# Kernel tuning notes

Hardware: AMD Instinct MI355X
Metric: run time of the kernel (lower is better)

The kernel has to match this reference:

```python
import jax, jax.numpy as jnp
import numpy as np

NEG_SLOPE = 0.01  # nn.LeakyReLU default
NUM_GRAPHS = 64


def leaky_relu(x):
    return jnp.where(x >= 0, x, NEG_SLOPE * x)


def gcn_conv(x, edge_index, W, b):
    """PyG GCNConv: add self-loops, symmetric norm, aggregate, + bias."""
    n = x.shape[0]
    h = x @ W  # [N, F]
    loop = jnp.arange(n, dtype=edge_index.dtype)
    src = jnp.concatenate([edge_index[0], loop])
    dst = jnp.concatenate([edge_index[1], loop])
    deg = jax.ops.segment_sum(jnp.ones_like(dst, dtype=h.dtype), dst, num_segments=n)
    dinv = jnp.where(deg > 0, deg ** -0.5, 0.0)
    norm = dinv[src] * dinv[dst]  # [E+N]
    msg = h[src] * norm[:, None]  # [E+N, F] dominant intermediate
    out = jax.ops.segment_sum(msg, dst, num_segments=n)
    return out + b


def gep(x, batch, num_graphs):
    """global mean pool over batch segment ids."""
    s = jax.ops.segment_sum(x, batch, num_segments=num_graphs)
    cnt = jax.ops.segment_sum(jnp.ones(x.shape[0], dtype=x.dtype), batch, num_segments=num_graphs)
    return s / jnp.maximum(cnt, 1.0)[:, None]


def setup_inputs() -> dict:
    key = jax.random.key(0)
    ks = jax.random.split(key, 16)
    N, E, F, D, B = 10000, 80000, 1024, 128, NUM_GRAPHS
    sc = 1.0 / np.sqrt(F)
    inp = {
        "pro1_x": jax.random.normal(ks[0], (N, F), jnp.float32),
        "pro1_edge_index": jax.random.randint(ks[1], (2, E), 0, N, jnp.int64),
        "pro1_batch": jnp.sort(jax.random.randint(ks[2], (N,), 0, B, jnp.int64)),
        "pro2_x": jax.random.normal(ks[3], (N, F), jnp.float32),
        "pro2_edge_index": jax.random.randint(ks[4], (2, E), 0, N, jnp.int64),
        "pro2_batch": jnp.sort(jax.random.randint(ks[5], (N,), 0, B, jnp.int64)),
        "mas1_straight": 0, "mas1_flipped": 0, "mas2_straight": 0, "mas2_flipped": 0,
        "conv1_W": jax.random.normal(ks[6], (F, F), jnp.float32) * sc,
        "conv1_b": jnp.zeros((F,), jnp.float32),
        "fc1_W": jax.random.normal(ks[7], (F, D), jnp.float32) * sc,
        "fc1_b": jnp.zeros((D,), jnp.float32),
        "conv2_W": jax.random.normal(ks[8], (F, F), jnp.float32) * sc,
        "conv2_b": jnp.zeros((F,), jnp.float32),
        "fc2_W": jax.random.normal(ks[9], (F, D), jnp.float32) * sc,
        "fc2_b": jnp.zeros((D,), jnp.float32),
        "final_W": jax.random.normal(ks[10], (2 * D, 1), jnp.float32) * (1.0 / np.sqrt(2 * D)),
        "final_b": jnp.zeros((1,), jnp.float32),
    }
    return inp


def reference(pro1_x, pro1_edge_index, pro1_batch, pro2_x, pro2_edge_index, pro2_batch,
              mas1_straight, mas1_flipped, mas2_straight, mas2_flipped,
              conv1_W, conv1_b, fc1_W, fc1_b, conv2_W, conv2_b, fc2_W, fc2_b,
              final_W, final_b):
    # branch 1 (dropout = identity at inference)
    x = leaky_relu(gcn_conv(pro1_x, pro1_edge_index, conv1_W, conv1_b))
    x = gep(x, pro1_batch, NUM_GRAPHS)
    x = leaky_relu(x @ fc1_W + fc1_b)
    # branch 2
    xt = leaky_relu(gcn_conv(pro2_x, pro2_edge_index, conv2_W, conv2_b))
    xt = gep(xt, pro2_batch, NUM_GRAPHS)
    xt = leaky_relu(xt @ fc2_W + fc2_b)
    combined = jnp.concatenate([x, xt], axis=1)  # [B, 256]
    return combined @ final_W + final_b  # [B, 1]
```

## Files before the change

kernel.cpp:

```cpp
#include <hip/hip_runtime.h>
#include <cstdint>
#include <cstddef>

#define FDIM 1024
#define DDIM 128
#define NGRAPH 64
#define FCH 8
#define QN 4

#define AS1 __attribute__((address_space(1)))
#define AS3 __attribute__((address_space(3)))

typedef float f32x4 __attribute__((ext_vector_type(4)));
typedef short s16x8 __attribute__((ext_vector_type(8)));

__device__ __forceinline__ unsigned short f2bf(float f) {
  unsigned int x = __float_as_uint(f);
  unsigned int r = (x + 0x7fffu + ((x >> 16) & 1u)) >> 16;
  return (unsigned short)r;
}
__device__ __forceinline__ float bf2f(unsigned short u) {
  return __uint_as_float(((unsigned int)u) << 16);
}
__device__ __forceinline__ float bflo(unsigned int v) {
  return __uint_as_float(v << 16);
}
__device__ __forceinline__ float bfhi(unsigned int v) {
  return __uint_as_float(v & 0xffff0000u);
}

__device__ __forceinline__ int lower_bound(const int* a, int n, int v) {
  int lo = 0, hi = n;
  while (lo < hi) {
    int mid = (lo + hi) >> 1;
    if (a[mid] < v) lo = mid + 1; else hi = mid;
  }
  return lo;
}
__global__ __launch_bounds__(256) void k_init_cnt(float4* pool1, float4* pool2,
                                                  int* deg1, int* deg2,
                                                  const int* __restrict__ batch1,
                                                  const int* __restrict__ batch2,
                                                  int* cnt1, int* gstart1,
                                                  int* cnt2, int* gstart2, int N) {
  int bid = blockIdx.x, t = threadIdx.x;
  const float4 z = make_float4(0.f, 0.f, 0.f, 0.f);
  if (bid < 64) {
    pool1[bid * 256 + t] = z;
  } else if (bid < 128) {
    pool2[(bid - 64) * 256 + t] = z;
  } else if (bid < 168) {
    int i = (bid - 128) * 256 + t;
    if (i < N) deg1[i] = 1;
  } else if (bid < 208) {
    int i = (bid - 168) * 256 + t;
    if (i < N) deg2[i] = 1;
  } else {
    if (t < 128) {
      const int* batch = (t < NGRAPH) ? batch1 : batch2;
      int* cnt = (t < NGRAPH) ? cnt1 : cnt2;
      int* gstart = (t < NGRAPH) ? gstart1 : gstart2;
      int g = t & (NGRAPH - 1);
      int lo = lower_bound(batch, N, g);
      int hi = lower_bound(batch, N, g + 1);
      gstart[g] = lo;
      cnt[g] = hi - lo;
    }
  }
}

__global__ void k_prep(const int* __restrict__ ei1, const int* __restrict__ ei2,
                       int* deg1, int* deg2, int E) {
  const int* ei = blockIdx.y ? ei2 : ei1;
  int* deg = blockIdx.y ? deg2 : deg1;
  int i = blockIdx.x * blockDim.x + threadIdx.x;
  if (i < E) atomicAdd(&deg[ei[E + i]], 1);
}

#define SCAN_T 1024
#define SCAN_PER 16
__global__ __launch_bounds__(SCAN_T) void k_scan(const int* __restrict__ deg1,
                                                 const int* __restrict__ deg2,
                                                 int* off1, int* off2,
                                                 int* cur1, int* cur2,
                                                 float* dinv1, float* dinv2, int n) {
  const int* deg = blockIdx.x ? deg2 : deg1;
  int* off = blockIdx.x ? off2 : off1;
  int* cur = blockIdx.x ? cur2 : cur1;
  float* dinv = blockIdx.x ? dinv2 : dinv1;
  __shared__ int sums[SCAN_T];
  int t = threadIdx.x;
  int base = t * SCAN_PER;
  int local[SCAN_PER];
  int s = 0;
  #pragma unroll
  for (int i = 0; i < SCAN_PER; ++i) {
    int idx = base + i;
    int d = (idx < n) ? deg[idx] : 0;
    local[i] = s;
    s += d;
    if (idx < n) dinv[idx] = rsqrtf((float)d);
  }
  sums[t] = s;
  __syncthreads();
  for (int o = 1; o < SCAN_T; o <<= 1) {
    int v = (t >= o) ? sums[t - o] : 0;
    __syncthreads();
    sums[t] += v;
    __syncthreads();
  }
  int basesum = (t > 0) ? sums[t - 1] : 0;
  #pragma unroll
  for (int i = 0; i < SCAN_PER; ++i) {
    int idx = base + i;
    if (idx < n) { int o = basesum + local[i]; off[idx] = o; cur[idx] = o; }
  }
  if (t == SCAN_T - 1) off[n] = sums[SCAN_T - 1];
}

__global__ void k_fill(const int* __restrict__ ei1, const int* __restrict__ ei2,
                       int* cur1, int* cur2,
                       const float* __restrict__ dinv1, const float* __restrict__ dinv2,
                       int* adjsrc1, int* adjsrc2,
                       float* adjw1, float* adjw2, int E, int N) {
  const int* ei = blockIdx.y ? ei2 : ei1;
  int* cur = blockIdx.y ? cur2 : cur1;
  const float* dinv = blockIdx.y ? dinv2 : dinv1;
  int* adjsrc = blockIdx.y ? adjsrc2 : adjsrc1;
  float* adjw = blockIdx.y ? adjw2 : adjw1;
  int i = blockIdx.x * blockDim.x + threadIdx.x;
  if (i < E) {
    int s = ei[i];
    int d = ei[E + i];
    int p = atomicAdd(&cur[d], 1);
    adjsrc[p] = s;
    adjw[p] = dinv[s] * dinv[d];
  }
  if (i < N) {
    int p = atomicAdd(&cur[i], 1);
    adjsrc[p] = i;
    adjw[p] = dinv[i] * dinv[i];
  }
}

__global__ __launch_bounds__(256) void k_cast(const float4* __restrict__ x1,
                                              const float4* __restrict__ x2,
                                              const float* __restrict__ W1,
                                              const float* __restrict__ W2,
                                              ushort4* xb1, ushort4* xb2,
                                              unsigned short* Wt1, unsigned short* Wt2,
                                              int n4, int nxb) {
  __shared__ unsigned short tile[64][65];
  int bid = blockIdx.x, t = threadIdx.x;
  if (bid < 2 * nxb) {
    int br = bid >= nxb;
    const float4* x = br ? x2 : x1;
    ushort4* xb = br ? xb2 : xb1;
    int i = (bid - br * nxb) * 256 + t;
    if (i < n4) {
      float4 v = x[i];
      ushort4 o;
      o.x = f2bf(v.x); o.y = f2bf(v.y); o.z = f2bf(v.z); o.w = f2bf(v.w);
      xb[i] = o;
    }
  } else {
    int w = bid - 2 * nxb;
    int br = w >= 256;
    const float* W = br ? W2 : W1;
    unsigned short* Wt = br ? Wt2 : Wt1;
    int tid16 = w - br * 256;
    int kb = tid16 >> 4, nb = tid16 & 15;
    int tn = t & 63, tg = t >> 6;
    #pragma unroll
    for (int r = 0; r < 16; ++r) {
      int kk = tg * 16 + r;
      tile[kk][tn] = f2bf(W[(size_t)(kb * 64 + kk) * FDIM + nb * 64 + tn]);
    }
    __syncthreads();
    #pragma unroll
    for (int r = 0; r < 16; ++r) {
      int nn = tg * 16 + r;
      Wt[(size_t)(nb * 64 + nn) * FDIM + kb * 64 + tn] = tile[tn][nn];
    }
  }
}

__global__ __launch_bounds__(256) void k_gemm_bf16(const unsigned short* __restrict__ A1,
                                                   const unsigned short* __restrict__ A2,
                                                   const unsigned short* __restrict__ B1,
                                                   const unsigned short* __restrict__ B2,
                                                   unsigned short* __restrict__ C1,
                                                   unsigned short* __restrict__ C2,
                                                   int M) {
  const unsigned short* A = blockIdx.y ? A2 : A1;
  const unsigned short* Bt = blockIdx.y ? B2 : B1;
  unsigned short* C = blockIdx.y ? C2 : C1;
  const int K = FDIM;
  __shared__ unsigned short sm[8192];
  int tid = threadIdx.x;
  int w = tid >> 6, lane = tid & 63;
  int wm = w >> 1, wn = w & 1;

  int per_xcd = gridDim.x >> 3;
  int l = (blockIdx.x & 7) * per_xcd + (blockIdx.x >> 3);
  int m0 = (l >> 3) * 128;
  int n0 = (l & 7) * 128;

  int sub = lane >> 2;
  int kq = lane & 3;

  f32x4 acc[4][4];
  #pragma unroll
  for (int i = 0; i < 4; ++i)
    #pragma unroll
    for (int j = 0; j < 4; ++j)
      acc[i][j] = (f32x4){0.f, 0.f, 0.f, 0.f};

  for (int k0 = 0; k0 < K; k0 += 32) {
    #pragma unroll
    for (int j = 0; j < 2; ++j) {
      int chunk = w * 2 + j;
      int ra = m0 + chunk * 16 + sub;
      if (ra > M - 1) ra = M - 1;
      const unsigned short* ga = A + (size_t)ra * K + k0 + kq * 8;
      __builtin_amdgcn_global_load_lds((const AS1 unsigned int*)ga,
                                       (AS3 unsigned int*)&sm[chunk * 512], 16, 0, 0);
      int rb = n0 + chunk * 16 + sub;
      const unsigned short* gb = Bt + (size_t)rb * K + k0 + kq * 8;
      __builtin_amdgcn_global_load_lds((const AS1 unsigned int*)gb,
                                       (AS3 unsigned int*)&sm[4096 + chunk * 512], 16, 0, 0);
    }
    __syncthreads();
    s16x8 af[4], bfr[4];
    #pragma unroll
    for (int i = 0; i < 4; ++i) {
      int rowa = wm * 64 + i * 16 + (lane & 15);
      af[i] = *(const s16x8*)&sm[rowa * 32 + (lane >> 4) * 8];
      int rowb = wn * 64 + i * 16 + (lane & 15);
      bfr[i] = *(const s16x8*)&sm[4096 + rowb * 32 + (lane >> 4) * 8];
    }
    #pragma unroll
    for (int i = 0; i < 4; ++i)
      #pragma unroll
      for (int j = 0; j < 4; ++j)
        acc[i][j] = __builtin_amdgcn_mfma_f32_16x16x32_bf16(af[i], bfr[j], acc[i][j], 0, 0, 0);
    __syncthreads();
  }

  #pragma unroll
  for (int i = 0; i < 4; ++i) {
    int row_base = m0 + wm * 64 + i * 16 + (lane >> 4) * 4;
    #pragma unroll
    for (int j = 0; j < 4; ++j) {
      int col = n0 + wn * 64 + j * 16 + (lane & 15);
      #pragma unroll
      for (int r = 0; r < 4; ++r) {
        int row = row_base + r;
        if (row < M) C[(size_t)row * FDIM + col] = f2bf(acc[i][j][r]);
      }
    }
  }
}

__global__ __launch_bounds__(256) void k_aggpool(const unsigned short* __restrict__ h1,
                                                 const unsigned short* __restrict__ h2,
                                                 const int* __restrict__ off1,
                                                 const int* __restrict__ off2,
                                                 const int* __restrict__ adjsrc1,
                                                 const int* __restrict__ adjsrc2,
                                                 const float* __restrict__ adjw1,
                                                 const float* __restrict__ adjw2,
                                                 const float* __restrict__ bias1,
                                                 const float* __restrict__ bias2,
                                                 const int* __restrict__ cnt1,
                                                 const int* __restrict__ cnt2,
                                                 const int* __restrict__ gstart1,
                                                 const int* __restrict__ gstart2,
                                                 float* pool1, float* pool2) {
  int br = blockIdx.y;
  const unsigned short* h = br ? h2 : h1;
  const int* off = br ? off2 : off1;
  const int* adjsrc = br ? adjsrc2 : adjsrc1;
  const float* adjw = br ? adjw2 : adjw1;
  const float* bias = br ? bias2 : bias1;
  const int* cnt = br ? cnt2 : cnt1;
  const int* gstart = br ? gstart2 : gstart1;
  float* pool = br ? pool2 : pool1;

  int x = blockIdx.x;
  int chunk = x & (FCH - 1);
  int r = x >> 3;
  int g = r & (NGRAPH - 1);
  int q = r >> 6;

  int t = threadIdx.x;
  int grp = t >> 6, lane = t & 63;

  int n = cnt[g];
  int start = gstart[g];
  int per = (n + QN - 1) / QN;
  int v0 = start + q * per;
  int v1 = min(start + n, v0 + per);

  int colbase = chunk * 128 + lane * 2;
  const unsigned short* hc = h + colbase;
  float2 b2 = *(const float2*)(bias + colbase);
  float s0 = 0.f, s1 = 0.f;

  for (int v = v0 + grp; v < v1; v += 4) {
    int pb = off[v], pe = off[v + 1];
    float a0 = 0.f, a1 = 0.f;
    for (int pbb = pb; pbb < pe; pbb += 64) {
      int m = min(64, pe - pbb);
      int lp = pbb + ((lane < m) ? lane : (m - 1));
      int vs = adjsrc[lp];
      float vw = adjw[lp];
      int j = 0;
      for (; j + 4 <= m; j += 4) {
        int i0 = __shfl(vs, j),     i1 = __shfl(vs, j + 1);
        int i2 = __shfl(vs, j + 2), i3 = __shfl(vs, j + 3);
        float w0 = __shfl(vw, j),     w1 = __shfl(vw, j + 1);
        float w2 = __shfl(vw, j + 2), w3 = __shfl(vw, j + 3);
        unsigned int h0 = *(const unsigned int*)(hc + ((size_t)i0 << 10));
        unsigned int hv1 = *(const unsigned int*)(hc + ((size_t)i1 << 10));
        unsigned int hv2 = *(const unsigned int*)(hc + ((size_t)i2 << 10));
        unsigned int hv3 = *(const unsigned int*)(hc + ((size_t)i3 << 10));
        a0 += w0 * bflo(h0);  a1 += w0 * bfhi(h0);
        a0 += w1 * bflo(hv1); a1 += w1 * bfhi(hv1);
        a0 += w2 * bflo(hv2); a1 += w2 * bfhi(hv2);
        a0 += w3 * bflo(hv3); a1 += w3 * bfhi(hv3);
      }
      for (; j < m; ++j) {
        int i0 = __shfl(vs, j);
        float w0 = __shfl(vw, j);
        unsigned int h0 = *(const unsigned int*)(hc + ((size_t)i0 << 10));
        a0 += w0 * bflo(h0);
        a1 += w0 * bfhi(h0);
      }
    }
    a0 += b2.x; a1 += b2.y;
    s0 += (a0 >= 0.f) ? a0 : 0.01f * a0;
    s1 += (a1 >= 0.f) ? a1 : 0.01f * a1;
  }

  __shared__ float sm[4][128];
  sm[grp][lane * 2] = s0;
  sm[grp][lane * 2 + 1] = s1;
  __syncthreads();
  if (t < 128) {
    float sum = sm[0][t] + sm[1][t] + sm[2][t] + sm[3][t];
    float ic = 1.0f / fmaxf((float)n, 1.0f);
    atomicAdd(pool + (size_t)g * FDIM + chunk * 128 + t, sum * ic);
  }
}

__global__ __launch_bounds__(DDIM) void k_fc(const float* __restrict__ pool1,
                                             const float* __restrict__ pool2,
                                             const float* __restrict__ W1,
                                             const float* __restrict__ W2,
                                             const float* __restrict__ b1,
                                             const float* __restrict__ b2,
                                             float* out1, float* out2) {
  const float* pool = blockIdx.y ? pool2 : pool1;
  const float* W = blockIdx.y ? W2 : W1;
  const float* b = blockIdx.y ? b2 : b1;
  float* out = blockIdx.y ? out2 : out1;
  int g = blockIdx.x;
  int j = threadIdx.x;
  __shared__ float xs[FDIM];
  for (int k = j; k < FDIM; k += DDIM) xs[k] = pool[(size_t)g * FDIM + k];
  __syncthreads();
  float acc = b[j];
  for (int k = 0; k < FDIM; ++k) acc += xs[k] * W[(size_t)k * DDIM + j];
  out[g * DDIM + j] = (acc >= 0.f) ? acc : 0.01f * acc;
}

__global__ __launch_bounds__(DDIM) void k_final(const float* __restrict__ o1,
                                                const float* __restrict__ o2,
                                                const float* __restrict__ W,
                                                const float* __restrict__ b,
                                                float* __restrict__ out) {
  int g = blockIdx.x;
  int t = threadIdx.x;
  float acc = o1[g * DDIM + t] * W[t] + o2[g * DDIM + t] * W[DDIM + t];
  #pragma unroll
  for (int o = 32; o > 0; o >>= 1) acc += __shfl_down(acc, o);
  __shared__ float ws2[2];
  if ((t & 63) == 0) ws2[t >> 6] = acc;
  __syncthreads();
  if (t == 0) out[g] = ws2[0] + ws2[1] + b[0];
}

extern "C" void kernel_launch(void* const* d_in, const int* in_sizes, int n_in,
                              void* d_out, int out_size, void* d_ws, size_t ws_size,
                              hipStream_t stream) {
  const float* x1 = (const float*)d_in[0];
  const int* ei1 = (const int*)d_in[1];
  const int* batch1 = (const int*)d_in[2];
  const float* x2 = (const float*)d_in[3];
  const int* ei2 = (const int*)d_in[4];
  const int* batch2 = (const int*)d_in[5];
  const float* conv1_W = (const float*)d_in[10];
  const float* conv1_b = (const float*)d_in[11];
  const float* fc1_W = (const float*)d_in[12];
  const float* fc1_b = (const float*)d_in[13];
  const float* conv2_W = (const float*)d_in[14];
  const float* conv2_b = (const float*)d_in[15];
  const float* fc2_W = (const float*)d_in[16];
  const float* fc2_b = (const float*)d_in[17];
  const float* final_W = (const float*)d_in[18];
  const float* final_b = (const float*)d_in[19];
  float* out = (float*)d_out;

  const int N = in_sizes[2];
  const int E = in_sizes[1] / 2;
  const int A = E + N;

  size_t off_b = 0;
  auto alloc = [&](size_t bytes) -> void* {
    void* p = (char*)d_ws + off_b;
    off_b += (bytes + 255) & ~(size_t)255;
    return p;
  };
  unsigned short* xbf1 = (unsigned short*)alloc((size_t)N * FDIM * 2);
  unsigned short* xbf2 = (unsigned short*)alloc((size_t)N * FDIM * 2);
  unsigned short* hbf1 = (unsigned short*)alloc((size_t)N * FDIM * 2);
  unsigned short* hbf2 = (unsigned short*)alloc((size_t)N * FDIM * 2);
  unsigned short* Wt1 = (unsigned short*)alloc((size_t)FDIM * FDIM * 2);
  unsigned short* Wt2 = (unsigned short*)alloc((size_t)FDIM * FDIM * 2);
  int* deg1 = (int*)alloc(N * 4);
  int* deg2 = (int*)alloc(N * 4);
  int* cnt1 = (int*)alloc(NGRAPH * 4);
  int* cnt2 = (int*)alloc(NGRAPH * 4);
  int* gstart1 = (int*)alloc(NGRAPH * 4);
  int* gstart2 = (int*)alloc(NGRAPH * 4);
  int* off1 = (int*)alloc((N + 1) * 4);
  int* off2 = (int*)alloc((N + 1) * 4);
  int* cur1 = (int*)alloc(N * 4);
  int* cur2 = (int*)alloc(N * 4);
  float* dinv1 = (float*)alloc(N * 4);
  float* dinv2 = (float*)alloc(N * 4);
  int* adjsrc1 = (int*)alloc((size_t)A * 4);
  int* adjsrc2 = (int*)alloc((size_t)A * 4);
  float* adjw1 = (float*)alloc((size_t)A * 4);
  float* adjw2 = (float*)alloc((size_t)A * 4);
  float* pool1 = (float*)alloc(NGRAPH * FDIM * 4);
  float* pool2 = (float*)alloc(NGRAPH * FDIM * 4);
  float* fco1 = (float*)alloc(NGRAPH * DDIM * 4);
  float* fco2 = (float*)alloc(NGRAPH * DDIM * 4);

  const int T = 256;
  int gE = (E + T - 1) / T;
  int n4 = N * FDIM / 4;
  int nxb = (n4 + T - 1) / T;
  int mt = (N + 127) / 128;
  dim3 gGemm(mt * 8, 2);
  dim3 gPrep(gE, 2);
  dim3 gAgg(FCH * NGRAPH * QN, 2);
  dim3 gFc(NGRAPH, 2);

  k_init_cnt<<<209, T, 0, stream>>>((float4*)pool1, (float4*)pool2, deg1, deg2,
                                    batch1, batch2, cnt1, gstart1, cnt2, gstart2, N);
  k_prep<<<gPrep, T, 0, stream>>>(ei1, ei2, deg1, deg2, E);
  k_scan<<<2, SCAN_T, 0, stream>>>(deg1, deg2, off1, off2, cur1, cur2, dinv1, dinv2, N);
  k_fill<<<gPrep, T, 0, stream>>>(ei1, ei2, cur1, cur2, dinv1, dinv2,
                                  adjsrc1, adjsrc2, adjw1, adjw2, E, N);
  k_cast<<<2 * nxb + 512, T, 0, stream>>>((const float4*)x1, (const float4*)x2,
                                          conv1_W, conv2_W,
                                          (ushort4*)xbf1, (ushort4*)xbf2, Wt1, Wt2,
                                          n4, nxb);
  k_gemm_bf16<<<gGemm, 256, 0, stream>>>(xbf1, xbf2, Wt1, Wt2, hbf1, hbf2, N);
  k_aggpool<<<gAgg, 256, 0, stream>>>(hbf1, hbf2, off1, off2, adjsrc1, adjsrc2,
                                      adjw1, adjw2, conv1_b, conv2_b,
                                      cnt1, cnt2, gstart1, gstart2, pool1, pool2);
  k_fc<<<gFc, DDIM, 0, stream>>>(pool1, pool2, fc1_W, fc2_W, fc1_b, fc2_b, fco1, fco2);
  k_final<<<NGRAPH, DDIM, 0, stream>>>(fco1, fco2, final_W, final_b, out);
}
```

Baseline: 340.5 us.

## Merge prep/cast and fill/gemm launches; replace pool atomics with per-quarter partials

Folds the degree-count atomics into the cast kernel and the CSR fill into the GEMM launch as extra leading blocks, which removes two kernel launches and lets the independent work run concurrently. The pooled-sum atomics are replaced by per-quarter partial buffers that k_fc reduces, so the pool zeroing in the init kernel can be dropped. The cost is larger grids with divergent block roles, a fixed FILLB block count that must cover E (320 blocks of 256 ≥ 80000), and extra partial-buffer memory.

```diff
diff --git a/kernel.cpp b/kernel.cpp
--- a/kernel.cpp
+++ b/kernel.cpp
@@ -7,6 +7,7 @@
 #define NGRAPH 64
 #define FCH 8
 #define QN 4
+#define FILLB 320
 
 #define AS1 __attribute__((address_space(1)))
 #define AS3 __attribute__((address_space(3)))
@@ -18,9 +19,6 @@
   unsigned int x = __float_as_uint(f);
   unsigned int r = (x + 0x7fffu + ((x >> 16) & 1u)) >> 16;
   return (unsigned short)r;
-}
-__device__ __forceinline__ float bf2f(unsigned short u) {
-  return __uint_as_float(((unsigned int)u) << 16);
 }
 __device__ __forceinline__ float bflo(unsigned int v) {
   return __uint_as_float(v << 16);
@@ -37,23 +35,17 @@
   }
   return lo;
 }
-__global__ __launch_bounds__(256) void k_init_cnt(float4* pool1, float4* pool2,
-                                                  int* deg1, int* deg2,
-                                                  const int* __restrict__ batch1,
-                                                  const int* __restrict__ batch2,
-                                                  int* cnt1, int* gstart1,
-                                                  int* cnt2, int* gstart2, int N) {
+__global__ __launch_bounds__(256) void k_init(int* deg1, int* deg2,
+                                              const int* __restrict__ batch1,
+                                              const int* __restrict__ batch2,
+                                              int* cnt1, int* gstart1,
+                                              int* cnt2, int* gstart2, int N) {
   int bid = blockIdx.x, t = threadIdx.x;
-  const float4 z = make_float4(0.f, 0.f, 0.f, 0.f);
-  if (bid < 64) {
-    pool1[bid * 256 + t] = z;
-  } else if (bid < 128) {
-    pool2[(bid - 64) * 256 + t] = z;
-  } else if (bid < 168) {
-    int i = (bid - 128) * 256 + t;
+  if (bid < 40) {
+    int i = bid * 256 + t;
     if (i < N) deg1[i] = 1;
-  } else if (bid < 208) {
-    int i = (bid - 168) * 256 + t;
+  } else if (bid < 80) {
+    int i = (bid - 40) * 256 + t;
     if (i < N) deg2[i] = 1;
   } else {
     if (t < 128) {
@@ -69,12 +61,52 @@
   }
 }
 
-__global__ void k_prep(const int* __restrict__ ei1, const int* __restrict__ ei2,
-                       int* deg1, int* deg2, int E) {
-  const int* ei = blockIdx.y ? ei2 : ei1;
-  int* deg = blockIdx.y ? deg2 : deg1;
-  int i = blockIdx.x * blockDim.x + threadIdx.x;
-  if (i < E) atomicAdd(&deg[ei[E + i]], 1);
+__global__ __launch_bounds__(256) void k_prep_cast(const int* __restrict__ ei1,
+                                                   const int* __restrict__ ei2,
+                                                   int* deg1, int* deg2,
+                                                   const float4* __restrict__ x1,
+                                                   const float4* __restrict__ x2,
+                                                   const float* __restrict__ W1,
+                                                   const float* __restrict__ W2,
+                                                   ushort4* xb1, ushort4* xb2,
+                                                   unsigned short* Wt1, unsigned short* Wt2,
+                                                   int E, int n4, int gE, int nxb) {
+  __shared__ unsigned short tile[64][65];
+  int br = blockIdx.y;
+  int x = blockIdx.x, t = threadIdx.x;
+  if (x < gE) {
+    const int* ei = br ? ei2 : ei1;
+    int* deg = br ? deg2 : deg1;
+    int i = x * 256 + t;
+    if (i < E) atomicAdd(&deg[ei[E + i]], 1);
+  } else if (x < gE + nxb) {
+    const float4* xx = br ? x2 : x1;
+    ushort4* xb = br ? xb2 : xb1;
+    int i = (x - gE) * 256 + t;
+    if (i < n4) {
+      float4 v = xx[i];
+      ushort4 o;
+      o.x = f2bf(v.x); o.y = f2bf(v.y); o.z = f2bf(v.z); o.w = f2bf(v.w);
+      xb[i] = o;
+    }
+  } else {
+    const float* W = br ? W2 : W1;
+    unsigned short* Wt = br ? Wt2 : Wt1;
+    int tid16 = x - gE - nxb;
+    int kb = tid16 >> 4, nb = tid16 & 15;
+    int tn = t & 63, tg = t >> 6;
+    #pragma unroll
+    for (int r = 0; r < 16; ++r) {
+      int kk = tg * 16 + r;
+      tile[kk][tn] = f2bf(W[(size_t)(kb * 64 + kk) * FDIM + nb * 64 + tn]);
+    }
+    __syncthreads();
+    #pragma unroll
+    for (int r = 0; r < 16; ++r) {
+      int nn = tg * 16 + r;
+      Wt[(size_t)(nb * 64 + nn) * FDIM + kb * 64 + tn] = tile[tn][nn];
+    }
+  }
 }
 
 #define SCAN_T 1024
@@ -118,91 +150,54 @@
   if (t == SCAN_T - 1) off[n] = sums[SCAN_T - 1];
 }
 
-__global__ void k_fill(const int* __restrict__ ei1, const int* __restrict__ ei2,
-                       int* cur1, int* cur2,
-                       const float* __restrict__ dinv1, const float* __restrict__ dinv2,
-                       int* adjsrc1, int* adjsrc2,
-                       float* adjw1, float* adjw2, int E, int N) {
-  const int* ei = blockIdx.y ? ei2 : ei1;
-  int* cur = blockIdx.y ? cur2 : cur1;
-  const float* dinv = blockIdx.y ? dinv2 : dinv1;
-  int* adjsrc = blockIdx.y ? adjsrc2 : adjsrc1;
-  float* adjw = blockIdx.y ? adjw2 : adjw1;
-  int i = blockIdx.x * blockDim.x + threadIdx.x;
-  if (i < E) {
-    int s = ei[i];
-    int d = ei[E + i];
-    int p = atomicAdd(&cur[d], 1);
-    adjsrc[p] = s;
-    adjw[p] = dinv[s] * dinv[d];
-  }
-  if (i < N) {
-    int p = atomicAdd(&cur[i], 1);
-    adjsrc[p] = i;
-    adjw[p] = dinv[i] * dinv[i];
-  }
-}
-
-__global__ __launch_bounds__(256) void k_cast(const float4* __restrict__ x1,
-                                              const float4* __restrict__ x2,
-                                              const float* __restrict__ W1,
-                                              const float* __restrict__ W2,
-                                              ushort4* xb1, ushort4* xb2,
-                                              unsigned short* Wt1, unsigned short* Wt2,
-                                              int n4, int nxb) {
-  __shared__ unsigned short tile[64][65];
-  int bid = blockIdx.x, t = threadIdx.x;
-  if (bid < 2 * nxb) {
-    int br = bid >= nxb;
-    const float4* x = br ? x2 : x1;
-    ushort4* xb = br ? xb2 : xb1;
-    int i = (bid - br * nxb) * 256 + t;
-    if (i < n4) {
-      float4 v = x[i];
-      ushort4 o;
-      o.x = f2bf(v.x); o.y = f2bf(v.y); o.z = f2bf(v.z); o.w = f2bf(v.w);
-      xb[i] = o;
-    }
-  } else {
-    int w = bid - 2 * nxb;
-    int br = w >= 256;
-    const float* W = br ? W2 : W1;
-    unsigned short* Wt = br ? Wt2 : Wt1;
-    int tid16 = w - br * 256;
-    int kb = tid16 >> 4, nb = tid16 & 15;
-    int tn = t & 63, tg = t >> 6;
-    #pragma unroll
-    for (int r = 0; r < 16; ++r) {
-      int kk = tg * 16 + r;
-      tile[kk][tn] = f2bf(W[(size_t)(kb * 64 + kk) * FDIM + nb * 64 + tn]);
-    }
-    __syncthreads();
-    #pragma unroll
-    for (int r = 0; r < 16; ++r) {
-      int nn = tg * 16 + r;
-      Wt[(size_t)(nb * 64 + nn) * FDIM + kb * 64 + tn] = tile[tn][nn];
-    }
-  }
-}
-
-__global__ __launch_bounds__(256) void k_gemm_bf16(const unsigned short* __restrict__ A1,
+__global__ __launch_bounds__(256) void k_fill_gemm(const int* __restrict__ ei1,
+                                                   const int* __restrict__ ei2,
+                                                   int* cur1, int* cur2,
+                                                   const float* __restrict__ dinv1,
+                                                   const float* __restrict__ dinv2,
+                                                   int* adjsrc1, int* adjsrc2,
+                                                   float* adjw1, float* adjw2,
+                                                   const unsigned short* __restrict__ A1,
                                                    const unsigned short* __restrict__ A2,
                                                    const unsigned short* __restrict__ B1,
                                                    const unsigned short* __restrict__ B2,
                                                    unsigned short* __restrict__ C1,
                                                    unsigned short* __restrict__ C2,
-                                                   int M) {
-  const unsigned short* A = blockIdx.y ? A2 : A1;
-  const unsigned short* Bt = blockIdx.y ? B2 : B1;
-  unsigned short* C = blockIdx.y ? C2 : C1;
+                                                   int E, int N, int M) {
+  __shared__ unsigned short sm[8192];
+  int br = blockIdx.y;
+  if (blockIdx.x < FILLB) {
+    const int* ei = br ? ei2 : ei1;
+    int* cur = br ? cur2 : cur1;
+    const float* dinv = br ? dinv2 : dinv1;
+    int* adjsrc = br ? adjsrc2 : adjsrc1;
+    float* adjw = br ? adjw2 : adjw1;
+    int i = blockIdx.x * 256 + threadIdx.x;
+    if (i < E) {
+      int s = ei[i];
+      int d = ei[E + i];
+      int p = atomicAdd(&cur[d], 1);
+      adjsrc[p] = s;
+      adjw[p] = dinv[s] * dinv[d];
+    }
+    if (i < N) {
+      int p = atomicAdd(&cur[i], 1);
+      adjsrc[p] = i;
+      adjw[p] = dinv[i] * dinv[i];
+    }
+    return;
+  }
+  const unsigned short* A = br ? A2 : A1;
+  const unsigned short* Bt = br ? B2 : B1;
+  unsigned short* C = br ? C2 : C1;
   const int K = FDIM;
-  __shared__ unsigned short sm[8192];
   int tid = threadIdx.x;
   int w = tid >> 6, lane = tid & 63;
   int wm = w >> 1, wn = w & 1;
 
-  int per_xcd = gridDim.x >> 3;
-  int l = (blockIdx.x & 7) * per_xcd + (blockIdx.x >> 3);
+  int bx = blockIdx.x - FILLB;
+  int per_xcd = (gridDim.x - FILLB) >> 3;
+  int l = (bx & 7) * per_xcd + (bx >> 3);
   int m0 = (l >> 3) * 128;
   int n0 = (l & 7) * 128;
 
@@ -276,7 +271,7 @@
                                                  const int* __restrict__ cnt2,
                                                  const int* __restrict__ gstart1,
                                                  const int* __restrict__ gstart2,
-                                                 float* pool1, float* pool2) {
+                                                 float* pool4_1, float* pool4_2) {
   int br = blockIdx.y;
   const unsigned short* h = br ? h2 : h1;
   const int* off = br ? off2 : off1;
@@ -285,7 +280,7 @@
   const float* bias = br ? bias2 : bias1;
   const int* cnt = br ? cnt2 : cnt1;
   const int* gstart = br ? gstart2 : gstart1;
-  float* pool = br ? pool2 : pool1;
+  float* pool4 = br ? pool4_2 : pool4_1;
 
   int x = blockIdx.x;
   int chunk = x & (FCH - 1);
@@ -350,25 +345,31 @@
   if (t < 128) {
     float sum = sm[0][t] + sm[1][t] + sm[2][t] + sm[3][t];
     float ic = 1.0f / fmaxf((float)n, 1.0f);
-    atomicAdd(pool + (size_t)g * FDIM + chunk * 128 + t, sum * ic);
-  }
-}
-
-__global__ __launch_bounds__(DDIM) void k_fc(const float* __restrict__ pool1,
-                                             const float* __restrict__ pool2,
+    pool4[((size_t)(q * NGRAPH + g)) * FDIM + chunk * 128 + t] = sum * ic;
+  }
+}
+
+__global__ __launch_bounds__(DDIM) void k_fc(const float* __restrict__ pool4_1,
+                                             const float* __restrict__ pool4_2,
                                              const float* __restrict__ W1,
                                              const float* __restrict__ W2,
                                              const float* __restrict__ b1,
                                              const float* __restrict__ b2,
                                              float* out1, float* out2) {
-  const float* pool = blockIdx.y ? pool2 : pool1;
+  const float* pool4 = blockIdx.y ? pool4_2 : pool4_1;
   const float* W = blockIdx.y ? W2 : W1;
   const float* b = blockIdx.y ? b2 : b1;
   float* out = blockIdx.y ? out2 : out1;
   int g = blockIdx.x;
   int j = threadIdx.x;
   __shared__ float xs[FDIM];
-  for (int k = j; k < FDIM; k += DDIM) xs[k] = pool[(size_t)g * FDIM + k];
+  for (int k = j; k < FDIM; k += DDIM) {
+    float v = 0.f;
+    #pragma unroll
+    for (int q = 0; q < QN; ++q)
+      v += pool4[((size_t)(q * NGRAPH + g)) * FDIM + k];
+    xs[k] = v;
+  }
   __syncthreads();
   float acc = b[j];
   for (int k = 0; k < FDIM; ++k) acc += xs[k] * W[(size_t)k * DDIM + j];
@@ -444,8 +445,8 @@
   int* adjsrc2 = (int*)alloc((size_t)A * 4);
   float* adjw1 = (float*)alloc((size_t)A * 4);
   float* adjw2 = (float*)alloc((size_t)A * 4);
-  float* pool1 = (float*)alloc(NGRAPH * FDIM * 4);
-  float* pool2 = (float*)alloc(NGRAPH * FDIM * 4);
+  float* pool4_1 = (float*)alloc((size_t)QN * NGRAPH * FDIM * 4);
+  float* pool4_2 = (float*)alloc((size_t)QN * NGRAPH * FDIM * 4);
   float* fco1 = (float*)alloc(NGRAPH * DDIM * 4);
   float* fco2 = (float*)alloc(NGRAPH * DDIM * 4);
 
@@ -454,25 +455,26 @@
   int n4 = N * FDIM / 4;
   int nxb = (n4 + T - 1) / T;
   int mt = (N + 127) / 128;
-  dim3 gGemm(mt * 8, 2);
-  dim3 gPrep(gE, 2);
+  dim3 gPrepCast(gE + nxb + 256, 2);
+  dim3 gFillGemm(FILLB + mt * 8, 2);
   dim3 gAgg(FCH * NGRAPH * QN, 2);
   dim3 gFc(NGRAPH, 2);
 
-  k_init_cnt<<<209, T, 0, stream>>>((float4*)pool1, (float4*)pool2, deg1, deg2,
-                                    batch1, batch2, cnt1, gstart1, cnt2, gstart2, N);
-  k_prep<<<gPrep, T, 0, stream>>>(ei1, ei2, deg1, deg2, E);
+  k_init<<<81, T, 0, stream>>>(deg1, deg2, batch1, batch2,
+                               cnt1, gstart1, cnt2, gstart2, N);
+  k_prep_cast<<<gPrepCast, T, 0, stream>>>(ei1, ei2, deg1, deg2,
+                                           (const float4*)x1, (const float4*)x2,
+                                           conv1_W, conv2_W,
+                                           (ushort4*)xbf1, (ushort4*)xbf2, Wt1, Wt2,
+                                           E, n4, gE, nxb);
   k_scan<<<2, SCAN_T, 0, stream>>>(deg1, deg2, off1, off2, cur1, cur2, dinv1, dinv2, N);
-  k_fill<<<gPrep, T, 0, stream>>>(ei1, ei2, cur1, cur2, dinv1, dinv2,
-                                  adjsrc1, adjsrc2, adjw1, adjw2, E, N);
-  k_cast<<<2 * nxb + 512, T, 0, stream>>>((const float4*)x1, (const float4*)x2,
-                                          conv1_W, conv2_W,
-                                          (ushort4*)xbf1, (ushort4*)xbf2, Wt1, Wt2,
-                                          n4, nxb);
-  k_gemm_bf16<<<gGemm, 256, 0, stream>>>(xbf1, xbf2, Wt1, Wt2, hbf1, hbf2, N);
-  k_aggpool<<<gAgg, 256, 0, stream>>>(hbf1, hbf2, off1, off2, adjsrc1, adjsrc2,
-                                      adjw1, adjw2, conv1_b, conv2_b,
-                                      cnt1, cnt2, gstart1, gstart2, pool1, pool2);
-  k_fc<<<gFc, DDIM, 0, stream>>>(pool1, pool2, fc1_W, fc2_W, fc1_b, fc2_b, fco1, fco2);
+  k_fill_gemm<<<gFillGemm, T, 0, stream>>>(ei1, ei2, cur1, cur2, dinv1, dinv2,
+                                           adjsrc1, adjsrc2, adjw1, adjw2,
+                                           xbf1, xbf2, Wt1, Wt2, hbf1, hbf2,
+                                           E, N, N);
+  k_aggpool<<<gAgg, T, 0, stream>>>(hbf1, hbf2, off1, off2, adjsrc1, adjsrc2,
+                                    adjw1, adjw2, conv1_b, conv2_b,
+                                    cnt1, cnt2, gstart1, gstart2, pool4_1, pool4_2);
+  k_fc<<<gFc, DDIM, 0, stream>>>(pool4_1, pool4_2, fc1_W, fc2_W, fc1_b, fc2_b, fco1, fco2);
   k_final<<<NGRAPH, DDIM, 0, stream>>>(fco1, fco2, final_W, final_b, out);
 }
```

New measurement: 333.1 us. 2.2% less time.
